# Performance work log

Hardware: AMD Instinct MI355X
Metric: run time of the kernel (lower is better)

Reference implementation:

```python
import jax, jax.numpy as jnp
import numpy as np

N = 16384; C = 16; H = 256; W = 704
HEADS = 4; PTS = 4; K = 8; DH = C // HEADS
EPS = 1e-3  # BatchNorm eps from module

def _bn(x, g, b):
    # BatchNorm1d in training mode: batch statistics over N
    mu = x.mean(axis=0)
    var = x.var(axis=0)
    return (x - mu) * jax.lax.rsqrt(var + EPS) * g + b

def setup_inputs():
    key = jax.random.key(0)
    ks = jax.random.split(key, 20)
    def w(i, shape, s=0.25):
        return jax.random.normal(ks[i], shape, jnp.float32) * s
    grid_y = jax.random.randint(ks[0], (N,), 0, H)
    grid_x = jax.random.randint(ks[1], (N,), 0, W)
    return {
        "point_features": jax.random.normal(ks[2], (N, C), jnp.float32),
        "image_feat": jax.random.normal(ks[3], (C, H, W), jnp.float32),
        "image_grid": jnp.stack([grid_y, grid_x], axis=1),
        "Wk": w(4, (C, C)), "bk": w(5, (C,)), "gk": jnp.ones((C,)), "betak": jnp.zeros((C,)),
        "Wfc": w(6, (2, C)), "bfc": w(7, (C,)), "gfc": jnp.ones((C,)), "betafc": jnp.zeros((C,)),
        "Wt": w(8, (C, C)), "bt": w(9, (C,)), "gt": jnp.ones((C,)), "betat": jnp.zeros((C,)),
        "Woff": w(10, (C, HEADS * PTS * 2), 0.02), "boff": w(11, (HEADS * PTS * 2,), 0.5),
        "Wattn": w(12, (C, HEADS * PTS), 0.02), "battn": jnp.zeros((HEADS * PTS,)),
        "Wval": w(13, (C, C)), "bval": w(14, (C,)),
        "Wout": w(15, (C, C)), "bout": w(16, (C,)),
        "Wf": w(17, (2 * C, C)), "bf": w(18, (C,)), "gf": jnp.ones((C,)), "betaf": jnp.zeros((C,)),
    }

def _deform_attn(q, image_feat, grid_f, Woff, boff, Wattn, battn, Wval, bval, Wout, bout):
    # MSDeformAttn with 1 level: learned offsets around projected pixel, bilinear sampling
    n = q.shape[0]
    off = (q @ Woff + boff).reshape(n, HEADS, PTS, 2)
    attn = jax.nn.softmax((q @ Wattn + battn).reshape(n, HEADS, PTS), axis=-1)
    val = (image_feat.reshape(C, H * W).T @ Wval + bval).reshape(H * W, HEADS, DH)
    val_h = val.transpose(1, 0, 2)  # [HEADS, HW, DH]
    loc_y = grid_f[:, 0][:, None, None] + off[..., 0]  # [N, HEADS, PTS]
    loc_x = grid_f[:, 1][:, None, None] + off[..., 1]
    y0 = jnp.floor(loc_y); x0 = jnp.floor(loc_x)
    wy = loc_y - y0; wx = loc_x - x0

    def corner(yi, xi, wgt):
        valid = (yi >= 0) & (yi <= H - 1) & (xi >= 0) & (xi <= W - 1)
        yc = jnp.clip(yi, 0, H - 1).astype(jnp.int32)
        xc = jnp.clip(xi, 0, W - 1).astype(jnp.int32)
        idx = (yc * W + xc).transpose(1, 0, 2)  # [HEADS, N, PTS]
        g = jax.vmap(lambda v, i: v[i])(val_h, idx)  # [HEADS, N, PTS, DH]
        return g * (wgt * valid).transpose(1, 0, 2)[..., None]

    samp = (corner(y0, x0, (1 - wy) * (1 - wx))
            + corner(y0, x0 + 1, (1 - wy) * wx)
            + corner(y0 + 1, x0, wy * (1 - wx))
            + corner(y0 + 1, x0 + 1, wy * wx))  # [HEADS, N, PTS, DH]
    out = (samp * attn.transpose(1, 0, 2)[..., None]).sum(axis=2)  # [HEADS, N, DH]
    out = out.transpose(1, 0, 2).reshape(n, C)
    return out @ Wout + bout

def reference(point_features, image_feat, image_grid, Wk, bk, gk, betak, Wfc, bfc, gfc, betafc, Wt, bt, gt, betat, Woff, boff, Wattn, battn, Wval, bval, Wout, bout, Wf, bf, gf, betaf):
    grid_f = image_grid.astype(jnp.float32)
    # KNN over projected pixel coords (cKDTree.query k=K+1, drop self)
    d2 = ((grid_f[:, None, :] - grid_f[None, :, :]) ** 2).sum(-1)
    _, nidx = jax.lax.top_k(-d2, K + 1)
    nidx = nidx[:, 1:]  # [N, K]

    pts = _bn(point_features @ Wk + bk, gk, betak)  # pts_key_proj
    # normalized relative image-plane positions -> fc
    center = grid_f.mean(axis=0)
    rel = grid_f - center
    mx = jnp.abs(rel).max(axis=0)
    mx = jnp.where(mx == 0, 1.0, mx)
    pos = _bn((rel / mx) @ Wfc + bfc, gfc, betafc)

    # gather image feats at projected pixels + KNN-graph neighbor aggregation
    gathered = image_feat[:, image_grid[:, 0], image_grid[:, 1]].T  # [N, C]
    neigh = gathered[nidx].mean(axis=1)  # [N, C]

    q = pts + pos
    img_pre = _deform_attn(q, image_feat, grid_f, Woff, boff, Wattn, battn, Wval, bval, Wout, bout) + neigh

    pts_pre = _bn(pts @ Wt + bt, gt, betat)  # pts_transform
    fuse = jax.nn.relu(jnp.concatenate([pts_pre, img_pre], axis=-1))  # activate_out
    return jax.nn.relu(_bn(fuse @ Wf + bf, gf, betaf))  # fuse_conv
```

## Files before the change

### kernel.cpp

```cpp
#include <hip/hip_runtime.h>
#include <climits>

#define N_ 16384
#define C_ 16
#define H_ 256
#define W_ 704
#define HW_ (H_*W_)
#define NC_ (N_*C_)
#define EPS_ 1e-3f
#define HDR_ 512

typedef unsigned long long ull;


#define VAL_   (HDR_ + 9*NC_)
#define KNNI_  (VAL_ + HW_*16)
#define PARTF_ (KNNI_ + 378256)
#define PK_    (PARTF_ + 8192)
#define PFC_   (PARTF_ + 16384)
#define PT_    (PARTF_ + 24576)

#define CAP_ 6144

__device__ __forceinline__ float wsum64(float v){
#pragma unroll
  for (int o = 32; o > 0; o >>= 1) v += __shfl_down(v, o);
  return v;
}

#define LOAD16(dst, src) { const float4* _s=(const float4*)(src); float4 _a=_s[0],_b=_s[1],_c=_s[2],_d=_s[3]; \
  dst[0]=_a.x;dst[1]=_a.y;dst[2]=_a.z;dst[3]=_a.w; dst[4]=_b.x;dst[5]=_b.y;dst[6]=_b.z;dst[7]=_b.w; \
  dst[8]=_c.x;dst[9]=_c.y;dst[10]=_c.z;dst[11]=_c.w; dst[12]=_d.x;dst[13]=_d.y;dst[14]=_d.z;dst[15]=_d.w; }

#define STORE16(dst, src) { float4* _d=(float4*)(dst); \
  _d[0]=make_float4(src[0],src[1],src[2],src[3]); _d[1]=make_float4(src[4],src[5],src[6],src[7]); \
  _d[2]=make_float4(src[8],src[9],src[10],src[11]); _d[3]=make_float4(src[12],src[13],src[14],src[15]); }

__global__ __launch_bounds__(256) void k_init(float* ws){
  if (blockIdx.x < 176){
    int4* c = (int4*)(ws + KNNI_);
    c[blockIdx.x*256 + threadIdx.x] = make_int4(0,0,0,0);
  } else if (threadIdx.x == 0){
    int* ih = (int*)ws;
    ih[0]=0; ih[1]=0; ih[2]=INT_MAX; ih[3]=INT_MIN; ih[4]=INT_MAX; ih[5]=INT_MIN;
  }
}

__global__ __launch_bounds__(256) void k_gridcnt(const int* __restrict__ grid, float* __restrict__ ws){
  int i = blockIdx.x*256 + threadIdx.x;
  int2 p = ((const int2*)grid)[i];
  int* counts = (int*)(ws + KNNI_);
  atomicAdd(&counts[p.x*W_ + p.y], 1);
  int sy=p.x, sx=p.y, mny=p.x, mxy=p.x, mnx=p.y, mxx=p.y;
#pragma unroll
  for (int o=32;o>0;o>>=1){
    sy += __shfl_down(sy,o); sx += __shfl_down(sx,o);
    mny = min(mny,__shfl_down(mny,o)); mxy = max(mxy,__shfl_down(mxy,o));
    mnx = min(mnx,__shfl_down(mnx,o)); mxx = max(mxx,__shfl_down(mxx,o));
  }
  __shared__ int sh[24];
  int w = threadIdx.x >> 6;
  if ((threadIdx.x & 63) == 0){
    sh[w]=sy; sh[4+w]=sx; sh[8+w]=mny; sh[12+w]=mxy; sh[16+w]=mnx; sh[20+w]=mxx;
  }
  __syncthreads();
  if (threadIdx.x == 0){
    int a0=sh[0]+sh[1]+sh[2]+sh[3];
    int a1=sh[4]+sh[5]+sh[6]+sh[7];
    int a2=min(min(sh[8],sh[9]),min(sh[10],sh[11]));
    int a3=max(max(sh[12],sh[13]),max(sh[14],sh[15]));
    int a4=min(min(sh[16],sh[17]),min(sh[18],sh[19]));
    int a5=max(max(sh[20],sh[21]),max(sh[22],sh[23]));
    int* ih = (int*)ws;
    atomicAdd(&ih[0],a0); atomicAdd(&ih[1],a1);
    atomicMin(&ih[2],a2); atomicMax(&ih[3],a3);
    atomicMin(&ih[4],a4); atomicMax(&ih[5],a5);
  }
}

__global__ __launch_bounds__(256) void k_scanA(float* ws){
  const int* counts = (const int*)(ws + KNNI_);
  int* bsum = (int*)(ws + KNNI_) + 180224 + 180240;
  int t = threadIdx.x;
  int v = counts[blockIdx.x*256 + t];
#pragma unroll
  for (int o=32;o>0;o>>=1) v += __shfl_down(v,o);
  __shared__ int w4[4];
  if ((t&63)==0) w4[t>>6] = v;
  __syncthreads();
  if (t==0) bsum[blockIdx.x] = w4[0]+w4[1]+w4[2]+w4[3];
}

__global__ __launch_bounds__(256) void k_scanB(float* ws){
  if (threadIdx.x == 0){
    int* ih = (int*)ws;
    float cy = (float)ih[0] / (float)N_;
    float cx = (float)ih[1] / (float)N_;
    float my = fmaxf((float)ih[3]-cy, cy-(float)ih[2]);
    float mx = fmaxf((float)ih[5]-cx, cx-(float)ih[4]);
    if (my == 0.f) my = 1.f;
    if (mx == 0.f) mx = 1.f;
    ws[264]=cy; ws[265]=cx; ws[266]=1.f/my; ws[267]=1.f/mx;
  }
  int* bsum = (int*)(ws + KNNI_) + 180224 + 180240;
  int* boff = bsum + 704;
  __shared__ int sWsum[4];
  __shared__ int sCarry;
  int t = threadIdx.x, lane = t & 63, wv = t >> 6;
  if (t==0) sCarry = 0;
  __syncthreads();
  for (int c=0;c<3;++c){
    int idx = c*256 + t;
    int v0 = (idx < 704) ? bsum[idx] : 0;
    int v = v0;
#pragma unroll
    for (int o=1;o<64;o<<=1){ int xx=__shfl_up(v,o); if (lane>=o) v+=xx; }
    if (lane==63) sWsum[wv]=v;
    __syncthreads();
    int add = sCarry;
    for (int w2=0;w2<wv;++w2) add += sWsum[w2];
    if (idx < 704) boff[idx] = add + v - v0;
    __syncthreads();
    if (t==255) sCarry = add + v;
    __syncthreads();
  }
}

__global__ __launch_bounds__(256) void k_scanC(float* ws){
  int* counts = (int*)(ws + KNNI_);
  int* cellst = counts + 180224;
  const int* boff = counts + 180224 + 180240 + 704;
  __shared__ int sWsum[4];
  int t = threadIdx.x, lane = t & 63, wv = t >> 6;
  int i = blockIdx.x*256 + t;
  int v0 = counts[i], v = v0;
#pragma unroll
  for (int o=1;o<64;o<<=1){ int xx=__shfl_up(v,o); if (lane>=o) v+=xx; }
  if (lane==63) sWsum[wv]=v;
  __syncthreads();
  int add = boff[blockIdx.x];
  for (int w2=0;w2<wv;++w2) add += sWsum[w2];
  int start = add + v - v0;
  cellst[i] = start;
  counts[i] = start;
  if (i == 0) cellst[HW_] = N_;
}

__global__ __launch_bounds__(256) void k_scatter(const int* __restrict__ grid, float* __restrict__ ws){
  int i = blockIdx.x*256 + threadIdx.x;
  int2 g = ((const int2*)grid)[i];
  int* counts = (int*)(ws + KNNI_);
  unsigned* psort = (unsigned*)(counts + 180224 + 180240 + 704 + 704);
  int pos = atomicAdd(&counts[g.x*W_ + g.y], 1);
  psort[pos] = ((unsigned)g.x<<24) | ((unsigned)g.y<<14) | (unsigned)i;
}

__global__ __launch_bounds__(256) void k_prep(const float* __restrict__ imf,
                                              const int* __restrict__ grid,
                                              const float* __restrict__ Wval,
                                              const float* __restrict__ bval,
                                              float* __restrict__ ws){
  int t = threadIdx.x;
  if (blockIdx.x < 1024){
    int idx = blockIdx.x*256 + t;
    int i = idx >> 4, c = idx & 15;
    int2 g = ((const int2*)grid)[i];
    ws[HDR_ + 2*NC_ + idx] = imf[c*HW_ + g.x*W_ + g.y];
  } else {
    __shared__ float sW[256], sb[16];
    sW[t] = Wval[t];
    if (t < 16) sb[t] = bval[t];
    __syncthreads();
    int pix = (blockIdx.x-1024)*256 + t;
    float a[16];
#pragma unroll
    for (int ci=0;ci<16;++ci) a[ci] = imf[ci*HW_ + pix];
    float o[16];
#pragma unroll
    for (int c=0;c<16;++c) o[c] = sb[c];
#pragma unroll
    for (int ci=0;ci<16;++ci){ float v=a[ci];
#pragma unroll
      for (int c=0;c<16;++c) o[c] += v*sW[ci*16+c];
    }
    float* val = ws + VAL_;
    STORE16(val + pix*16, o);
  }
}

__device__ __forceinline__ void knn_insert(ull* arr, ull key){
  if (key < arr[8]){
    int q = 8;
    while (q > 0 && arr[q-1] > key){ arr[q] = arr[q-1]; --q; }
    arr[q] = key;
  }
}

__device__ __forceinline__ void scan_rows_global(const int* __restrict__ cellst,
                                                 const unsigned* __restrict__ psort,
                                                 int y, int x, int s,
                                                 int y0, int y1, int x0, int x1, ull* arr){
  for (int yy=y0+s; yy<=y1; yy+=4){
    int rowb = yy*W_;
    int st = cellst[rowb + x0];
    int e  = cellst[rowb + x1 + 1];
    int dy = y-yy, dy2 = dy*dy;
    for (int p=st; p<e; ++p){
      unsigned u = psort[p];
      int px = (int)((u>>14)&1023);
      int dx = x-px;
      knn_insert(arr, ((ull)(unsigned)(dy2+dx*dx) << 14) | (ull)(u & 16383u));
    }
  }
}

__global__ __launch_bounds__(256) void k_knn4(float* __restrict__ ws){
  const int* cellst = (const int*)(ws + KNNI_) + 180224;
  const unsigned* psort = (const unsigned*)((const int*)(ws + KNNI_) + 180224 + 180240 + 704 + 704);
  __shared__ unsigned sBand[CAP_];
  __shared__ int sRowBase[80];
  __shared__ int sMn, sMx;
  int tid = threadIdx.x, lane = tid & 63;
  int s = tid & 3, pl = tid >> 2;
  int gid = blockIdx.x*64 + pl;
  unsigned me = psort[gid];
  int y = (int)(me>>24), x = (int)((me>>14)&1023), i = (int)(me&16383);
  if (tid==0){ sMn = INT_MAX; sMx = -1; }
  __syncthreads();
  if (s==0){ atomicMin(&sMn, y); atomicMax(&sMx, y); }
  __syncthreads();
  int ya = max(sMn-16,0), yb = min(sMx+16,H_-1);
  int nr = yb-ya+1;
  int p0 = cellst[ya*W_], p1 = cellst[(yb+1)*W_];
  int count = p1-p0;
  bool fb = (count > CAP_) || (nr > 78);
  if (!fb){
    for (int j=tid; j<count; j+=256) sBand[j] = psort[p0+j];
    for (int j=tid; j<=nr; j+=256) sRowBase[j] = cellst[(ya+j)*W_] - p0;
  }
  __syncthreads();
  int r = 8;
  { int y0=max(y-8,0),y1=min(y+8,H_-1),x0=max(x-8,0),x1=min(x+8,W_-1);
    if ((y1-y0+1)*(x1-x0+1) < 224) r = 16; }
  ull arr[9];
#pragma unroll
  for (int q=0;q<9;++q) arr[q] = ~0ull;
  {
    int y0=max(y-r,0),y1=min(y+r,H_-1),x0=max(x-r,0),x1=min(x+r,W_-1);
    if (!fb){
      for (int yy=y0+s; yy<=y1; yy+=4){
        int j = yy-ya;
        int b = sRowBase[j], e = sRowBase[j+1];
        int lo=b, hi=e;
        while (lo<hi){ int mid=(lo+hi)>>1; int xm=(int)((sBand[mid]>>14)&1023); if (xm<x0) lo=mid+1; else hi=mid; }
        int dy = y-yy, dy2 = dy*dy;
        for (int p=lo; p<e; ++p){
          unsigned u = sBand[p];
          int px = (int)((u>>14)&1023);
          if (px > x1) break;
          int dx = x-px;
          knn_insert(arr, ((ull)(unsigned)(dy2+dx*dx) << 14) | (ull)(u & 16383u));
        }
      }
    } else {
      scan_rows_global(cellst, psort, y, x, s, y0, y1, x0, x1, arr);
    }
  }
  ull m[9];
  bool done = false;
  {
    ull k[9];
#pragma unroll
    for (int q=0;q<9;++q) m[q] = ~0ull;
    int base = lane & ~3;
    for (int ss=0; ss<4; ++ss){
#pragma unroll
      for (int q=0;q<9;++q) k[q] = __shfl(arr[q], base+ss);
      for (int q2=0;q2<9;++q2){
        ull kk = k[q2];
        if (kk >= m[8]) break;
        int q = 8; while (q>0 && m[q-1]>kk){ m[q]=m[q-1]; --q; } m[q]=kk;
      }
    }
    int y0=max(y-r,0),y1=min(y+r,H_-1),x0=max(x-r,0),x1=min(x+r,W_-1);
    bool covered = (y0==0)&&(y1==H_-1)&&(x0==0)&&(x1==W_-1);
    bool ok = covered;
    if (!ok && m[8] != ~0ull){ int d9 = (int)(m[8]>>14); ok = d9 < (r+1)*(r+1); }
    done = ok;
  }
  while (__ballot(!done)){
    if (!done){
      r <<= 1;
      int y0=max(y-r,0),y1=min(y+r,H_-1),x0=max(x-r,0),x1=min(x+r,W_-1);
#pragma unroll
      for (int q=0;q<9;++q) arr[q] = ~0ull;
      scan_rows_global(cellst, psort, y, x, s, y0, y1, x0, x1, arr);
    }
    ull k[9];
    bool doIns = !done;
    if (doIns){
#pragma unroll
      for (int q=0;q<9;++q) m[q] = ~0ull;
    }
    int base = lane & ~3;
    for (int ss=0; ss<4; ++ss){
#pragma unroll
      for (int q=0;q<9;++q) k[q] = __shfl(arr[q], base+ss);
      if (doIns){
        for (int q2=0;q2<9;++q2){
          ull kk = k[q2];
          if (kk >= m[8]) break;
          int q = 8; while (q>0 && m[q-1]>kk){ m[q]=m[q-1]; --q; } m[q]=kk;
        }
      }
    }
    if (!done){
      int y0=max(y-r,0),y1=min(y+r,H_-1),x0=max(x-r,0),x1=min(x+r,W_-1);
      bool covered = (y0==0)&&(y1==H_-1)&&(x0==0)&&(x1==W_-1);
      bool ok = covered;
      if (!ok && m[8] != ~0ull){ int d9 = (int)(m[8]>>14); ok = d9 < (r+1)*(r+1); }
      if (ok) done = true;
    }
  }
  const float* gath = ws + HDR_ + 2*NC_;
  float4 acc = make_float4(0.f,0.f,0.f,0.f);
#pragma unroll
  for (int nb=1; nb<9; ++nb){
    int idx = (int)(m[nb] & 16383ull);
    const float4 g = *(const float4*)(gath + idx*16 + s*4);
    acc.x += g.x; acc.y += g.y; acc.z += g.z; acc.w += g.w;
  }
  float* neigh = ws + HDR_ + 7*NC_;
  *(float4*)(neigh + i*16 + s*4) =
      make_float4(acc.x*0.125f, acc.y*0.125f, acc.z*0.125f, acc.w*0.125f);
}

__global__ __launch_bounds__(64) void k_lin1(
    const float* __restrict__ pf, const int* __restrict__ grid,
    const float* __restrict__ Wk, const float* __restrict__ bk,
    const float* __restrict__ Wfc, const float* __restrict__ bfc,
    float* __restrict__ ws)
{
  __shared__ float sWk[256], sbk[16], sWfc[32], sbfc[16];
  int t = threadIdx.x;
  for (int j=t;j<256;j+=64) sWk[j] = Wk[j];
  if (t < 16){ sbk[t]=bk[t]; sbfc[t]=bfc[t]; }
  if (t < 32) sWfc[t] = Wfc[t];
  __syncthreads();
  int i = blockIdx.x*64 + t;
  float p[16]; LOAD16(p, pf + i*16);
  float ok[16];
#pragma unroll
  for (int c=0;c<16;++c) ok[c] = sbk[c];
#pragma unroll
  for (int j=0;j<16;++j){ float v = p[j];
#pragma unroll
    for (int c=0;c<16;++c) ok[c] += v*sWk[j*16+c];
  }
  float* pts_lin = ws + HDR_;
  STORE16(pts_lin + i*16, ok);
  float cy=ws[264], cx=ws[265], imy=ws[266], imx=ws[267];
  int2 g = ((const int2*)grid)[i];
  float ry = ((float)g.x - cy)*imy, rx = ((float)g.y - cx)*imx;
  float op[16];
#pragma unroll
  for (int c=0;c<16;++c) op[c] = ry*sWfc[c] + rx*sWfc[16+c] + sbfc[c];
  float* pos_lin = ws + HDR_ + NC_;
  STORE16(pos_lin + i*16, op);
  float* partK  = ws + PK_;
  float* partFC = ws + PFC_;
#pragma unroll
  for (int c=0;c<16;++c){
    float a = wsum64(ok[c]); float b = wsum64(ok[c]*ok[c]);
    if (t==0){ partK[blockIdx.x*32+c]=a; partK[blockIdx.x*32+16+c]=b; }
    a = wsum64(op[c]); b = wsum64(op[c]*op[c]);
    if (t==0){ partFC[blockIdx.x*32+c]=a; partFC[blockIdx.x*32+16+c]=b; }
  }
}

__device__ __forceinline__ void red1_body(const float* __restrict__ g, const float* __restrict__ b,
                                          float* __restrict__ ws, int partOff, int aOff, float* red){
  int t = threadIdx.x, slot = t & 31, chunk = t >> 5;
  const float* part = ws + partOff;
  float acc = 0.f;
  for (int bb=chunk*32; bb<chunk*32+32; ++bb) acc += part[bb*32 + slot];
  red[t] = acc;
  __syncthreads();
  if (chunk == 0){
    float v = red[slot];
#pragma unroll
    for (int k2=1;k2<8;++k2) v += red[k2*32+slot];
    red[slot] = v;
  }
  __syncthreads();
  if (t < 16){
    float mu  = red[t]    * (1.f/N_);
    float var = red[16+t] * (1.f/N_) - mu*mu;
    float a = g[t] / sqrtf(var + EPS_);
    ws[aOff+t]    = a;
    ws[aOff+16+t] = b[t] - mu*a;
  }
  __syncthreads();
}

__global__ __launch_bounds__(256) void k_red2(const float* __restrict__ gk, const float* __restrict__ betak,
                                              const float* __restrict__ gfc, const float* __restrict__ betafc,
                                              float* __restrict__ ws){
  __shared__ float red[256];
  red1_body(gk, betak, ws, PK_, 136, red);
  red1_body(gfc, betafc, ws, PFC_, 168, red);
}

__global__ __launch_bounds__(256) void k_red1(const float* __restrict__ g, const float* __restrict__ b,
                                              float* __restrict__ ws, int partOff, int aOff){
  __shared__ float red[256];
  red1_body(g, b, ws, partOff, aOff, red);
}

__global__ __launch_bounds__(64) void k_qstage(
    const float* __restrict__ Wt, const float* __restrict__ bt,
    const float* __restrict__ Woff, const float* __restrict__ boff,
    const float* __restrict__ Wattn, const float* __restrict__ battn,
    float* __restrict__ ws)
{
  __shared__ float sWt[256], sWoff[512], sWattn[256];
  __shared__ float sbt[16], sboff[32], sbattn[16];
  __shared__ float skA[16], skC[16], sfcA[16], sfcC[16];
  int t = threadIdx.x;
  for (int j=t;j<256;j+=64){ sWt[j]=Wt[j]; sWattn[j]=Wattn[j]; }
  for (int j=t;j<512;j+=64) sWoff[j]=Woff[j];
  if (t<16){ sbt[t]=bt[t]; sbattn[t]=battn[t];
    skA[t]=ws[136+t]; skC[t]=ws[152+t]; sfcA[t]=ws[168+t]; sfcC[t]=ws[184+t]; }
  if (t<32) sboff[t]=boff[t];
  __syncthreads();
  int i = blockIdx.x*64 + t;
  float* pts_lin = ws + HDR_;
  float* pos_lin = ws + HDR_ + NC_;
  float* t_lin   = ws + HDR_ + 3*NC_;
  float* offp    = ws + HDR_ + 4*NC_;
  float* attnp   = ws + HDR_ + 6*NC_;
  float pl[16], po[16];
  LOAD16(pl, pts_lin + i*16);
  LOAD16(po, pos_lin + i*16);
  float pts[16], q[16];
#pragma unroll
  for (int c=0;c<16;++c){ pts[c] = pl[c]*skA[c]+skC[c]; q[c] = pts[c] + po[c]*sfcA[c]+sfcC[c]; }
  float tv[16];
#pragma unroll
  for (int c=0;c<16;++c) tv[c] = sbt[c];
#pragma unroll
  for (int j=0;j<16;++j){ float v=pts[j];
#pragma unroll
    for (int c=0;c<16;++c) tv[c] += v*sWt[j*16+c];
  }
  STORE16(t_lin + i*16, tv);
  float* partT = ws + PT_;
#pragma unroll
  for (int c=0;c<16;++c){
    float a = wsum64(tv[c]); float b = wsum64(tv[c]*tv[c]);
    if (t==0){ partT[blockIdx.x*32+c]=a; partT[blockIdx.x*32+16+c]=b; }
  }
  float ov[32];
#pragma unroll
  for (int o=0;o<32;++o) ov[o] = sboff[o];
#pragma unroll
  for (int j=0;j<16;++j){ float v=q[j];
#pragma unroll
    for (int o=0;o<32;++o) ov[o] += v*sWoff[j*32+o];
  }
  { float4* d=(float4*)(offp + i*32);
#pragma unroll
    for (int r=0;r<8;++r) d[r]=make_float4(ov[r*4],ov[r*4+1],ov[r*4+2],ov[r*4+3]);
  }
  float l[16];
#pragma unroll
  for (int c=0;c<16;++c) l[c] = sbattn[c];
#pragma unroll
  for (int j=0;j<16;++j){ float v=q[j];
#pragma unroll
    for (int c=0;c<16;++c) l[c] += v*sWattn[j*16+c];
  }
  float av[16];
#pragma unroll
  for (int h=0;h<4;++h){
    float m = fmaxf(fmaxf(l[h*4],l[h*4+1]),fmaxf(l[h*4+2],l[h*4+3]));
    float e0=expf(l[h*4]-m), e1=expf(l[h*4+1]-m), e2=expf(l[h*4+2]-m), e3=expf(l[h*4+3]-m);
    float inv = 1.f/(e0+e1+e2+e3);
    av[h*4]=e0*inv; av[h*4+1]=e1*inv; av[h*4+2]=e2*inv; av[h*4+3]=e3*inv;
  }
  STORE16(attnp + i*16, av);
}

__global__ __launch_bounds__(256) void k_attn(
    const int* __restrict__ grid,
    const float* __restrict__ Wout, const float* __restrict__ bout,
    const float* __restrict__ Wf, const float* __restrict__ bf,
    float* __restrict__ ws)
{
  __shared__ float sWout[256], sWf[512], sbout[16], sbf[16];
  __shared__ float sTl[1024], sNei[1024], sSamp[1024], sImg[1024];
  __shared__ float sPart[128];
  int t = threadIdx.x;
  int p = t >> 2, h = t & 3;
  int i = blockIdx.x*64 + p;
  sWout[t]=Wout[t]; sWf[t]=Wf[t]; sWf[t+256]=Wf[t+256];
  if (t<16){ sbout[t]=bout[t]; sbf[t]=bf[t]; }
  {
    const float4* tl4 = (const float4*)(ws + HDR_ + 3*NC_ + blockIdx.x*1024);
    const float4* nv4 = (const float4*)(ws + HDR_ + 7*NC_ + blockIdx.x*1024);
    float4 v = tl4[t];
    int c0 = (t*4) & 15;
    float a0=ws[200+c0],a1=ws[200+c0+1],a2=ws[200+c0+2],a3=ws[200+c0+3];
    float c0v=ws[216+c0],c1v=ws[216+c0+1],c2v=ws[216+c0+2],c3v=ws[216+c0+3];
    sTl[t*4]   = fmaxf(v.x*a0+c0v, 0.f);
    sTl[t*4+1] = fmaxf(v.y*a1+c1v, 0.f);
    sTl[t*4+2] = fmaxf(v.z*a2+c2v, 0.f);
    sTl[t*4+3] = fmaxf(v.w*a3+c3v, 0.f);
    float4 nv = nv4[t];
    sNei[t*4]=nv.x; sNei[t*4+1]=nv.y; sNei[t*4+2]=nv.z; sNei[t*4+3]=nv.w;
  }
  const float4* off4 = (const float4*)(ws + HDR_ + 4*NC_ + blockIdx.x*2048);
  float4 o0 = off4[t*2], o1 = off4[t*2+1];
  float4 aw = ((const float4*)(ws + HDR_ + 6*NC_ + blockIdx.x*1024))[t];
  int2 g = ((const int2*)grid)[i];
  float y = (float)g.x, x = (float)g.y;
  const float4* val4 = (const float4*)(ws + VAL_);
  float4 acc = make_float4(0.f,0.f,0.f,0.f);
  float offv[8] = {o0.x,o0.y,o0.z,o0.w,o1.x,o1.y,o1.z,o1.w};
  float avv[4]  = {aw.x,aw.y,aw.z,aw.w};
#define CORNER(yy,xx,wgt) do{ int _y=(yy),_x=(xx); \
    if ((unsigned)_y < (unsigned)H_ && (unsigned)_x < (unsigned)W_){ \
      float4 _v = val4[(_y*W_+_x)*4 + h]; float _w = a*(wgt); \
      acc.x += _w*_v.x; acc.y += _w*_v.y; acc.z += _w*_v.z; acc.w += _w*_v.w; } }while(0)
#pragma unroll
  for (int pt=0; pt<4; ++pt){
    float a  = avv[pt];
    float ly = y + offv[pt*2], lx = x + offv[pt*2+1];
    float fy = floorf(ly), fx = floorf(lx);
    float wy = ly - fy, wx = lx - fx;
    int y0 = (int)fy, x0 = (int)fx;
    CORNER(y0,   x0,   (1.f-wy)*(1.f-wx));
    CORNER(y0,   x0+1, (1.f-wy)*wx);
    CORNER(y0+1, x0,   wy*(1.f-wx));
    CORNER(y0+1, x0+1, wy*wx);
  }
#undef CORNER
  ((float4*)sSamp)[t] = acc;
  __syncthreads();
  float img[4];
#pragma unroll
  for (int k=0;k<4;++k){ int cc=h*4+k; img[k] = sbout[cc] + sNei[p*16+cc]; }
#pragma unroll
  for (int j=0;j<16;++j){
    float v = sSamp[p*16+j];
#pragma unroll
    for (int k=0;k<4;++k) img[k] += v*sWout[j*16 + h*4 + k];
  }
  ((float4*)sImg)[t] = make_float4(img[0],img[1],img[2],img[3]);
  __syncthreads();
  float fl[4];
#pragma unroll
  for (int k=0;k<4;++k) fl[k] = sbf[h*4+k];
#pragma unroll
  for (int j=0;j<16;++j){
    float v1 = sTl[p*16+j];
    float v2 = fmaxf(sImg[p*16+j], 0.f);
#pragma unroll
    for (int k=0;k<4;++k){
      fl[k] += v1*sWf[j*16 + h*4 + k];
      fl[k] += v2*sWf[(16+j)*16 + h*4 + k];
    }
  }
  float* f_lin = ws + HDR_ + 8*NC_;
  ((float4*)(f_lin + blockIdx.x*1024))[t] = make_float4(fl[0],fl[1],fl[2],fl[3]);
  float s0=fl[0],s1=fl[1],s2=fl[2],s3=fl[3];
  float q0=fl[0]*fl[0],q1=fl[1]*fl[1],q2=fl[2]*fl[2],q3=fl[3]*fl[3];
#pragma unroll
  for (int o=32;o>=4;o>>=1){
    s0+=__shfl_down(s0,o); s1+=__shfl_down(s1,o); s2+=__shfl_down(s2,o); s3+=__shfl_down(s3,o);
    q0+=__shfl_down(q0,o); q1+=__shfl_down(q1,o); q2+=__shfl_down(q2,o); q3+=__shfl_down(q3,o);
  }
  int wave = t >> 6, lane = t & 63;
  if (lane < 4){
    sPart[wave*32 + lane*4+0]=s0; sPart[wave*32 + lane*4+1]=s1;
    sPart[wave*32 + lane*4+2]=s2; sPart[wave*32 + lane*4+3]=s3;
    sPart[wave*32 + 16 + lane*4+0]=q0; sPart[wave*32 + 16 + lane*4+1]=q1;
    sPart[wave*32 + 16 + lane*4+2]=q2; sPart[wave*32 + 16 + lane*4+3]=q3;
  }
  __syncthreads();
  if (t < 32){
    float v = sPart[t]+sPart[32+t]+sPart[64+t]+sPart[96+t];
    (ws + PARTF_)[blockIdx.x*32 + t] = v;
  }
}

__global__ __launch_bounds__(256) void k_out(const float* __restrict__ ws, float* __restrict__ out){
  int idx = blockIdx.x*256 + threadIdx.x;
  int c = idx & 15;
  float v = ws[HDR_ + 8*NC_ + idx];
  out[idx] = fmaxf(v*ws[232+c] + ws[248+c], 0.f);
}

extern "C" void kernel_launch(void* const* d_in, const int* in_sizes, int n_in,
                              void* d_out, int out_size, void* d_ws, size_t ws_size,
                              hipStream_t stream)
{
  const float* pf    = (const float*)d_in[0];
  const float* imf   = (const float*)d_in[1];
  const int*   gridp = (const int*)d_in[2];
  const float* Wk   =(const float*)d_in[3],  *bk   =(const float*)d_in[4];
  const float* gk   =(const float*)d_in[5],  *betak=(const float*)d_in[6];
  const float* Wfc  =(const float*)d_in[7],  *bfc  =(const float*)d_in[8];
  const float* gfc  =(const float*)d_in[9],  *betafc=(const float*)d_in[10];
  const float* Wt   =(const float*)d_in[11], *bt   =(const float*)d_in[12];
  const float* gt   =(const float*)d_in[13], *betat=(const float*)d_in[14];
  const float* Woff =(const float*)d_in[15], *boff =(const float*)d_in[16];
  const float* Wattn=(const float*)d_in[17], *battn=(const float*)d_in[18];
  const float* Wval =(const float*)d_in[19], *bval =(const float*)d_in[20];
  const float* Wout =(const float*)d_in[21], *bout =(const float*)d_in[22];
  const float* Wf   =(const float*)d_in[23], *bf   =(const float*)d_in[24];
  const float* gf   =(const float*)d_in[25], *betaf=(const float*)d_in[26];
  float* ws  = (float*)d_ws;
  float* out = (float*)d_out;

  hipLaunchKernelGGL(k_init,     dim3(177),      dim3(256), 0, stream, ws);
  hipLaunchKernelGGL(k_gridcnt,  dim3(N_/256),   dim3(256), 0, stream, gridp, ws);
  hipLaunchKernelGGL(k_scanA,    dim3(704),      dim3(256), 0, stream, ws);
  hipLaunchKernelGGL(k_scanB,    dim3(1),        dim3(256), 0, stream, ws);
  hipLaunchKernelGGL(k_scanC,    dim3(704),      dim3(256), 0, stream, ws);
  hipLaunchKernelGGL(k_scatter,  dim3(N_/256),   dim3(256), 0, stream, gridp, ws);
  hipLaunchKernelGGL(k_prep,     dim3(1728),     dim3(256), 0, stream, imf, gridp, Wval, bval, ws);
  hipLaunchKernelGGL(k_lin1,     dim3(N_/64),    dim3(64),  0, stream, pf, gridp, Wk, bk, Wfc, bfc, ws);
  hipLaunchKernelGGL(k_red2,     dim3(1),        dim3(256), 0, stream, gk, betak, gfc, betafc, ws);
  hipLaunchKernelGGL(k_qstage,   dim3(N_/64),    dim3(64),  0, stream, Wt, bt, Woff, boff, Wattn, battn, ws);
  hipLaunchKernelGGL(k_red1,     dim3(1),        dim3(256), 0, stream, gt, betat, ws, PT_, 200);
  hipLaunchKernelGGL(k_knn4,     dim3(N_/64),    dim3(256), 0, stream, ws);
  hipLaunchKernelGGL(k_attn,     dim3(N_/64),    dim3(256), 0, stream, gridp, Wout, bout, Wf, bf, ws);
  hipLaunchKernelGGL(k_red1,     dim3(1),        dim3(256), 0, stream, gf, betaf, ws, PARTF_, 232);
  hipLaunchKernelGGL(k_out,      dim3(NC_/256),  dim3(256), 0, stream, ws, out);
}
```

Baseline: 224.4 us.

## Merge fifteen launches into eight by co-scheduling independent stages in block ranges

Independent stages (counting-grid init, point projections, gather, value projection, scans, BN reductions, KNN, query stage) now share kernels, each stage taking its own range of block indices. The single-block scan and final BN reductions become last-block-done patterns driven by atomic counters and thread fences. The output kernel is vectorized to float4. The aim is to cut launch overhead and serialization from many tiny kernels, at the cost of more complex inter-block synchronization that depends on correct fence semantics.

Result: slower. 230.8 us (+2.9%).

```diff
diff --git a/kernel.cpp b/kernel.cpp
--- a/kernel.cpp
+++ b/kernel.cpp
@@ -2,16 +2,14 @@
 #include <climits>
 
 #define N_ 16384
-#define C_ 16
 #define H_ 256
 #define W_ 704
 #define HW_ (H_*W_)
-#define NC_ (N_*C_)
+#define NC_ (N_*16)
 #define EPS_ 1e-3f
 #define HDR_ 512
 
 typedef unsigned long long ull;
-
 
 #define VAL_   (HDR_ + 9*NC_)
 #define KNNI_  (VAL_ + HW_*16)
@@ -35,158 +33,6 @@
 #define STORE16(dst, src) { float4* _d=(float4*)(dst); \
   _d[0]=make_float4(src[0],src[1],src[2],src[3]); _d[1]=make_float4(src[4],src[5],src[6],src[7]); \
   _d[2]=make_float4(src[8],src[9],src[10],src[11]); _d[3]=make_float4(src[12],src[13],src[14],src[15]); }
-
-__global__ __launch_bounds__(256) void k_init(float* ws){
-  if (blockIdx.x < 176){
-    int4* c = (int4*)(ws + KNNI_);
-    c[blockIdx.x*256 + threadIdx.x] = make_int4(0,0,0,0);
-  } else if (threadIdx.x == 0){
-    int* ih = (int*)ws;
-    ih[0]=0; ih[1]=0; ih[2]=INT_MAX; ih[3]=INT_MIN; ih[4]=INT_MAX; ih[5]=INT_MIN;
-  }
-}
-
-__global__ __launch_bounds__(256) void k_gridcnt(const int* __restrict__ grid, float* __restrict__ ws){
-  int i = blockIdx.x*256 + threadIdx.x;
-  int2 p = ((const int2*)grid)[i];
-  int* counts = (int*)(ws + KNNI_);
-  atomicAdd(&counts[p.x*W_ + p.y], 1);
-  int sy=p.x, sx=p.y, mny=p.x, mxy=p.x, mnx=p.y, mxx=p.y;
-#pragma unroll
-  for (int o=32;o>0;o>>=1){
-    sy += __shfl_down(sy,o); sx += __shfl_down(sx,o);
-    mny = min(mny,__shfl_down(mny,o)); mxy = max(mxy,__shfl_down(mxy,o));
-    mnx = min(mnx,__shfl_down(mnx,o)); mxx = max(mxx,__shfl_down(mxx,o));
-  }
-  __shared__ int sh[24];
-  int w = threadIdx.x >> 6;
-  if ((threadIdx.x & 63) == 0){
-    sh[w]=sy; sh[4+w]=sx; sh[8+w]=mny; sh[12+w]=mxy; sh[16+w]=mnx; sh[20+w]=mxx;
-  }
-  __syncthreads();
-  if (threadIdx.x == 0){
-    int a0=sh[0]+sh[1]+sh[2]+sh[3];
-    int a1=sh[4]+sh[5]+sh[6]+sh[7];
-    int a2=min(min(sh[8],sh[9]),min(sh[10],sh[11]));
-    int a3=max(max(sh[12],sh[13]),max(sh[14],sh[15]));
-    int a4=min(min(sh[16],sh[17]),min(sh[18],sh[19]));
-    int a5=max(max(sh[20],sh[21]),max(sh[22],sh[23]));
-    int* ih = (int*)ws;
-    atomicAdd(&ih[0],a0); atomicAdd(&ih[1],a1);
-    atomicMin(&ih[2],a2); atomicMax(&ih[3],a3);
-    atomicMin(&ih[4],a4); atomicMax(&ih[5],a5);
-  }
-}
-
-__global__ __launch_bounds__(256) void k_scanA(float* ws){
-  const int* counts = (const int*)(ws + KNNI_);
-  int* bsum = (int*)(ws + KNNI_) + 180224 + 180240;
-  int t = threadIdx.x;
-  int v = counts[blockIdx.x*256 + t];
-#pragma unroll
-  for (int o=32;o>0;o>>=1) v += __shfl_down(v,o);
-  __shared__ int w4[4];
-  if ((t&63)==0) w4[t>>6] = v;
-  __syncthreads();
-  if (t==0) bsum[blockIdx.x] = w4[0]+w4[1]+w4[2]+w4[3];
-}
-
-__global__ __launch_bounds__(256) void k_scanB(float* ws){
-  if (threadIdx.x == 0){
-    int* ih = (int*)ws;
-    float cy = (float)ih[0] / (float)N_;
-    float cx = (float)ih[1] / (float)N_;
-    float my = fmaxf((float)ih[3]-cy, cy-(float)ih[2]);
-    float mx = fmaxf((float)ih[5]-cx, cx-(float)ih[4]);
-    if (my == 0.f) my = 1.f;
-    if (mx == 0.f) mx = 1.f;
-    ws[264]=cy; ws[265]=cx; ws[266]=1.f/my; ws[267]=1.f/mx;
-  }
-  int* bsum = (int*)(ws + KNNI_) + 180224 + 180240;
-  int* boff = bsum + 704;
-  __shared__ int sWsum[4];
-  __shared__ int sCarry;
-  int t = threadIdx.x, lane = t & 63, wv = t >> 6;
-  if (t==0) sCarry = 0;
-  __syncthreads();
-  for (int c=0;c<3;++c){
-    int idx = c*256 + t;
-    int v0 = (idx < 704) ? bsum[idx] : 0;
-    int v = v0;
-#pragma unroll
-    for (int o=1;o<64;o<<=1){ int xx=__shfl_up(v,o); if (lane>=o) v+=xx; }
-    if (lane==63) sWsum[wv]=v;
-    __syncthreads();
-    int add = sCarry;
-    for (int w2=0;w2<wv;++w2) add += sWsum[w2];
-    if (idx < 704) boff[idx] = add + v - v0;
-    __syncthreads();
-    if (t==255) sCarry = add + v;
-    __syncthreads();
-  }
-}
-
-__global__ __launch_bounds__(256) void k_scanC(float* ws){
-  int* counts = (int*)(ws + KNNI_);
-  int* cellst = counts + 180224;
-  const int* boff = counts + 180224 + 180240 + 704;
-  __shared__ int sWsum[4];
-  int t = threadIdx.x, lane = t & 63, wv = t >> 6;
-  int i = blockIdx.x*256 + t;
-  int v0 = counts[i], v = v0;
-#pragma unroll
-  for (int o=1;o<64;o<<=1){ int xx=__shfl_up(v,o); if (lane>=o) v+=xx; }
-  if (lane==63) sWsum[wv]=v;
-  __syncthreads();
-  int add = boff[blockIdx.x];
-  for (int w2=0;w2<wv;++w2) add += sWsum[w2];
-  int start = add + v - v0;
-  cellst[i] = start;
-  counts[i] = start;
-  if (i == 0) cellst[HW_] = N_;
-}
-
-__global__ __launch_bounds__(256) void k_scatter(const int* __restrict__ grid, float* __restrict__ ws){
-  int i = blockIdx.x*256 + threadIdx.x;
-  int2 g = ((const int2*)grid)[i];
-  int* counts = (int*)(ws + KNNI_);
-  unsigned* psort = (unsigned*)(counts + 180224 + 180240 + 704 + 704);
-  int pos = atomicAdd(&counts[g.x*W_ + g.y], 1);
-  psort[pos] = ((unsigned)g.x<<24) | ((unsigned)g.y<<14) | (unsigned)i;
-}
-
-__global__ __launch_bounds__(256) void k_prep(const float* __restrict__ imf,
-                                              const int* __restrict__ grid,
-                                              const float* __restrict__ Wval,
-                                              const float* __restrict__ bval,
-                                              float* __restrict__ ws){
-  int t = threadIdx.x;
-  if (blockIdx.x < 1024){
-    int idx = blockIdx.x*256 + t;
-    int i = idx >> 4, c = idx & 15;
-    int2 g = ((const int2*)grid)[i];
-    ws[HDR_ + 2*NC_ + idx] = imf[c*HW_ + g.x*W_ + g.y];
-  } else {
-    __shared__ float sW[256], sb[16];
-    sW[t] = Wval[t];
-    if (t < 16) sb[t] = bval[t];
-    __syncthreads();
-    int pix = (blockIdx.x-1024)*256 + t;
-    float a[16];
-#pragma unroll
-    for (int ci=0;ci<16;++ci) a[ci] = imf[ci*HW_ + pix];
-    float o[16];
-#pragma unroll
-    for (int c=0;c<16;++c) o[c] = sb[c];
-#pragma unroll
-    for (int ci=0;ci<16;++ci){ float v=a[ci];
-#pragma unroll
-      for (int c=0;c<16;++c) o[c] += v*sW[ci*16+c];
-    }
-    float* val = ws + VAL_;
-    STORE16(val + pix*16, o);
-  }
-}
 
 __device__ __forceinline__ void knn_insert(ull* arr, ull key){
   if (key < arr[8]){
@@ -214,304 +60,479 @@
   }
 }
 
-__global__ __launch_bounds__(256) void k_knn4(float* __restrict__ ws){
-  const int* cellst = (const int*)(ws + KNNI_) + 180224;
-  const unsigned* psort = (const unsigned*)((const int*)(ws + KNNI_) + 180224 + 180240 + 704 + 704);
-  __shared__ unsigned sBand[CAP_];
-  __shared__ int sRowBase[80];
-  __shared__ int sMn, sMx;
-  int tid = threadIdx.x, lane = tid & 63;
-  int s = tid & 3, pl = tid >> 2;
-  int gid = blockIdx.x*64 + pl;
-  unsigned me = psort[gid];
-  int y = (int)(me>>24), x = (int)((me>>14)&1023), i = (int)(me&16383);
-  if (tid==0){ sMn = INT_MAX; sMx = -1; }
-  __syncthreads();
-  if (s==0){ atomicMin(&sMn, y); atomicMax(&sMx, y); }
-  __syncthreads();
-  int ya = max(sMn-16,0), yb = min(sMx+16,H_-1);
-  int nr = yb-ya+1;
-  int p0 = cellst[ya*W_], p1 = cellst[(yb+1)*W_];
-  int count = p1-p0;
-  bool fb = (count > CAP_) || (nr > 78);
-  if (!fb){
-    for (int j=tid; j<count; j+=256) sBand[j] = psort[p0+j];
-    for (int j=tid; j<=nr; j+=256) sRowBase[j] = cellst[(ya+j)*W_] - p0;
-  }
-  __syncthreads();
-  int r = 8;
-  { int y0=max(y-8,0),y1=min(y+8,H_-1),x0=max(x-8,0),x1=min(x+8,W_-1);
-    if ((y1-y0+1)*(x1-x0+1) < 224) r = 16; }
-  ull arr[9];
-#pragma unroll
-  for (int q=0;q<9;++q) arr[q] = ~0ull;
-  {
-    int y0=max(y-r,0),y1=min(y+r,H_-1),x0=max(x-r,0),x1=min(x+r,W_-1);
+__device__ __forceinline__ void red_body(const float* __restrict__ g, const float* __restrict__ bta,
+                                         const float* __restrict__ part, float* __restrict__ coef,
+                                         float* __restrict__ red){
+  int t = threadIdx.x, slot = t & 31, chunk = t >> 5;
+  float acc = 0.f;
+  for (int bb=chunk*32; bb<chunk*32+32; ++bb) acc += part[bb*32 + slot];
+  red[t] = acc;
+  __syncthreads();
+  if (chunk == 0){
+    float v = red[slot];
+#pragma unroll
+    for (int k2=1;k2<8;++k2) v += red[k2*32+slot];
+    red[slot] = v;
+  }
+  __syncthreads();
+  if (t < 16){
+    float mu  = red[t]    * (1.f/N_);
+    float var = red[16+t] * (1.f/N_) - mu*mu;
+    float a = g[t] / sqrtf(var + EPS_);
+    coef[t]    = a;
+    coef[16+t] = bta[t] - mu*a;
+  }
+  __syncthreads();
+}
+
+__global__ __launch_bounds__(256) void k1(const float* __restrict__ pf,
+                                          const float* __restrict__ imf,
+                                          const int* __restrict__ grid,
+                                          const float* __restrict__ Wk, const float* __restrict__ bk,
+                                          const float* __restrict__ Wval, const float* __restrict__ bval,
+                                          float* __restrict__ ws){
+  __shared__ float sA[256], sB[16];
+  const int t = threadIdx.x, b = blockIdx.x;
+  const bool ldsK = (b >= 177 && b < 241);
+  const bool ldsV = (b >= 1265);
+  if (ldsK){ sA[t] = Wk[t];   if (t < 16) sB[t] = bk[t]; }
+  if (ldsV){ sA[t] = Wval[t]; if (t < 16) sB[t] = bval[t]; }
+  if (ldsK || ldsV) __syncthreads();
+
+  if (b < 176){
+    int4* c4 = (int4*)(ws + KNNI_);
+    c4[b*256 + t] = make_int4(0,0,0,0);
+  } else if (b == 176){
+    if (t == 0){
+      int* ih = (int*)ws;
+      ih[0]=0; ih[1]=0; ih[2]=INT_MAX; ih[3]=INT_MIN; ih[4]=INT_MAX; ih[5]=INT_MIN;
+      ih[6]=0; ih[7]=0;
+    }
+  } else if (ldsK){
+    const int i = (b-177)*256 + t;
+    float p[16]; LOAD16(p, pf + i*16);
+    float ok[16];
+#pragma unroll
+    for (int c=0;c<16;++c) ok[c] = sB[c];
+#pragma unroll
+    for (int j=0;j<16;++j){ float v = p[j];
+#pragma unroll
+      for (int c=0;c<16;++c) ok[c] += v*sA[j*16+c];
+    }
+    STORE16(ws + HDR_ + i*16, ok);
+    float* partK = ws + PK_;
+    const int grp = i >> 6;
+#pragma unroll
+    for (int c=0;c<16;++c){
+      float a = wsum64(ok[c]); float q2 = wsum64(ok[c]*ok[c]);
+      if ((t&63)==0){ partK[grp*32+c]=a; partK[grp*32+16+c]=q2; }
+    }
+  } else if (b < 1265){
+    const int idx = (b-241)*256 + t;
+    const int i = idx >> 4, c = idx & 15;
+    int2 g = ((const int2*)grid)[i];
+    ws[HDR_ + 2*NC_ + idx] = imf[c*HW_ + g.x*W_ + g.y];
+  } else {
+    const int pix = (b-1265)*256 + t;
+    float a[16];
+#pragma unroll
+    for (int ci=0;ci<16;++ci) a[ci] = imf[ci*HW_ + pix];
+    float o[16];
+#pragma unroll
+    for (int c=0;c<16;++c) o[c] = sB[c];
+#pragma unroll
+    for (int ci=0;ci<16;++ci){ float v=a[ci];
+#pragma unroll
+      for (int c=0;c<16;++c) o[c] += v*sA[ci*16+c];
+    }
+    STORE16(ws + VAL_ + pix*16, o);
+  }
+}
+
+__global__ __launch_bounds__(256) void k2(const int* __restrict__ grid,
+                                          const float* __restrict__ gk, const float* __restrict__ betak,
+                                          float* __restrict__ ws){
+  const int t = threadIdx.x, b = blockIdx.x;
+  if (b < 64){
+    int i = b*256 + t;
+    int2 p = ((const int2*)grid)[i];
+    int* counts = (int*)(ws + KNNI_);
+    atomicAdd(&counts[p.x*W_ + p.y], 1);
+    int sy=p.x, sx=p.y, mny=p.x, mxy=p.x, mnx=p.y, mxx=p.y;
+#pragma unroll
+    for (int o=32;o>0;o>>=1){
+      sy += __shfl_down(sy,o); sx += __shfl_down(sx,o);
+      mny = min(mny,__shfl_down(mny,o)); mxy = max(mxy,__shfl_down(mxy,o));
+      mnx = min(mnx,__shfl_down(mnx,o)); mxx = max(mxx,__shfl_down(mxx,o));
+    }
+    __shared__ int sh[24];
+    int w = t >> 6;
+    if ((t & 63) == 0){
+      sh[w]=sy; sh[4+w]=sx; sh[8+w]=mny; sh[12+w]=mxy; sh[16+w]=mnx; sh[20+w]=mxx;
+    }
+    __syncthreads();
+    if (t == 0){
+      int a0=sh[0]+sh[1]+sh[2]+sh[3];
+      int a1=sh[4]+sh[5]+sh[6]+sh[7];
+      int a2=min(min(sh[8],sh[9]),min(sh[10],sh[11]));
+      int a3=max(max(sh[12],sh[13]),max(sh[14],sh[15]));
+      int a4=min(min(sh[16],sh[17]),min(sh[18],sh[19]));
+      int a5=max(max(sh[20],sh[21]),max(sh[22],sh[23]));
+      int* ih = (int*)ws;
+      atomicAdd(&ih[0],a0); atomicAdd(&ih[1],a1);
+      atomicMin(&ih[2],a2); atomicMax(&ih[3],a3);
+      atomicMin(&ih[4],a4); atomicMax(&ih[5],a5);
+    }
+  } else {
+    __shared__ float red[256];
+    red_body(gk, betak, ws + PK_, ws + 136, red);
+  }
+}
+
+__global__ __launch_bounds__(256) void k3(const float* __restrict__ Wt, const float* __restrict__ bt,
+                                          float* __restrict__ ws){
+  const int t = threadIdx.x, b = blockIdx.x;
+  int* ih = (int*)ws;
+  int* counts = (int*)(ws + KNNI_);
+  int* bsum   = counts + 360464;
+  int* boffp  = bsum + 704;
+  if (b < 704){
+    __shared__ int w4[4];
+    __shared__ int sWin;
+    int v = counts[b*256 + t];
+#pragma unroll
+    for (int o=32;o>0;o>>=1) v += __shfl_down(v,o);
+    if ((t&63)==0) w4[t>>6] = v;
+    __syncthreads();
+    if (t == 0){
+      bsum[b] = w4[0]+w4[1]+w4[2]+w4[3];
+      __threadfence();
+      int old = atomicAdd(&ih[6], 1);
+      sWin = (old == 703) ? 1 : 0;
+    }
+    __syncthreads();
+    if (sWin){
+      if (t == 0) __threadfence();
+      __syncthreads();
+      if (t == 0){
+        float cy = (float)ih[0] / (float)N_;
+        float cx = (float)ih[1] / (float)N_;
+        float my = fmaxf((float)ih[3]-cy, cy-(float)ih[2]);
+        float mx = fmaxf((float)ih[5]-cx, cx-(float)ih[4]);
+        if (my == 0.f) my = 1.f;
+        if (mx == 0.f) mx = 1.f;
+        ws[264]=cy; ws[265]=cx; ws[266]=1.f/my; ws[267]=1.f/mx;
+      }
+      __shared__ int sWsum[4];
+      __shared__ int sCarry;
+      int lane = t & 63, wv = t >> 6;
+      if (t==0) sCarry = 0;
+      __syncthreads();
+      for (int c=0;c<3;++c){
+        int idx = c*256 + t;
+        int v0 = (idx < 704) ? bsum[idx] : 0;
+        int vv = v0;
+#pragma unroll
+        for (int o=1;o<64;o<<=1){ int xx=__shfl_up(vv,o); if (lane>=o) vv+=xx; }
+        if (lane==63) sWsum[wv]=vv;
+        __syncthreads();
+        int add = sCarry;
+        for (int w2=0;w2<wv;++w2) add += sWsum[w2];
+        if (idx < 704) boffp[idx] = add + vv - v0;
+        __syncthreads();
+        if (t==255) sCarry = add + vv;
+        __syncthreads();
+      }
+    }
+  } else {
+    __shared__ float sWt[256];
+    sWt[t] = Wt[t];
+    __syncthreads();
+    const int i = (b-704)*256 + t;
+    float kA[16], kC[16];
+    LOAD16(kA, ws+136); LOAD16(kC, ws+152);
+    float pl[16]; LOAD16(pl, ws + HDR_ + i*16);
+    float pts[16];
+#pragma unroll
+    for (int c=0;c<16;++c) pts[c] = pl[c]*kA[c] + kC[c];
+    float tv[16];
+#pragma unroll
+    for (int c=0;c<16;++c) tv[c] = bt[c];
+#pragma unroll
+    for (int j=0;j<16;++j){ float v = pts[j];
+#pragma unroll
+      for (int c=0;c<16;++c) tv[c] += v*sWt[j*16+c];
+    }
+    STORE16(ws + HDR_ + 3*NC_ + i*16, tv);
+    float* partT = ws + PT_;
+    const int grp = i >> 6;
+#pragma unroll
+    for (int c=0;c<16;++c){
+      float a = wsum64(tv[c]); float q2 = wsum64(tv[c]*tv[c]);
+      if ((t&63)==0){ partT[grp*32+c]=a; partT[grp*32+16+c]=q2; }
+    }
+  }
+}
+
+__global__ __launch_bounds__(256) void k4(const int* __restrict__ grid,
+                                          const float* __restrict__ Wfc, const float* __restrict__ bfc,
+                                          const float* __restrict__ gt, const float* __restrict__ betat,
+                                          float* __restrict__ ws){
+  const int t = threadIdx.x, b = blockIdx.x;
+  int* counts = (int*)(ws + KNNI_);
+  int* cellst = counts + 180224;
+  int* bsum   = counts + 360464;
+  int* boffp  = bsum + 704;
+  if (b < 704){
+    __shared__ int sWsum[4];
+    int lane = t & 63, wv = t >> 6;
+    int i = b*256 + t;
+    int v0 = counts[i], v = v0;
+#pragma unroll
+    for (int o=1;o<64;o<<=1){ int xx=__shfl_up(v,o); if (lane>=o) v+=xx; }
+    if (lane==63) sWsum[wv]=v;
+    __syncthreads();
+    int add = boffp[b];
+    for (int w2=0;w2<wv;++w2) add += sWsum[w2];
+    int start = add + v - v0;
+    cellst[i] = start;
+    counts[i] = start;
+    if (i == 0) cellst[HW_] = N_;
+  } else if (b < 768){
+    const int i = (b-704)*256 + t;
+    float cy=ws[264], cx=ws[265], imy=ws[266], imx=ws[267];
+    int2 g = ((const int2*)grid)[i];
+    float ry = ((float)g.x - cy)*imy, rx = ((float)g.y - cx)*imx;
+    float op[16];
+#pragma unroll
+    for (int c=0;c<16;++c) op[c] = ry*Wfc[c] + rx*Wfc[16+c] + bfc[c];
+    STORE16(ws + HDR_ + NC_ + i*16, op);
+    float* partFC = ws + PFC_;
+    const int grp = i >> 6;
+#pragma unroll
+    for (int c=0;c<16;++c){
+      float a = wsum64(op[c]); float q2 = wsum64(op[c]*op[c]);
+      if ((t&63)==0){ partFC[grp*32+c]=a; partFC[grp*32+16+c]=q2; }
+    }
+  } else {
+    __shared__ float red[256];
+    red_body(gt, betat, ws + PT_, ws + 200, red);
+  }
+}
+
+__global__ __launch_bounds__(256) void k5(const int* __restrict__ grid,
+                                          const float* __restrict__ gfc, const float* __restrict__ betafc,
+                                          float* __restrict__ ws){
+  const int t = threadIdx.x, b = blockIdx.x;
+  if (b < 64){
+    int i = b*256 + t;
+    int2 g = ((const int2*)grid)[i];
+    int* counts = (int*)(ws + KNNI_);
+    unsigned* psort = (unsigned*)(counts + 180224 + 180240 + 704 + 704);
+    int pos = atomicAdd(&counts[g.x*W_ + g.y], 1);
+    psort[pos] = ((unsigned)g.x<<24) | ((unsigned)g.y<<14) | (unsigned)i;
+  } else {
+    __shared__ float red[256];
+    red_body(gfc, betafc, ws + PFC_, ws + 168, red);
+  }
+}
+
+__global__ __launch_bounds__(256) void k6(const float* __restrict__ WoffW, const float* __restrict__ boffW,
+                                          const float* __restrict__ Wattn, const float* __restrict__ battn,
+                                          float* __restrict__ ws){
+  const int t = threadIdx.x, b = blockIdx.x;
+  if (b < 256){
+    const int* cellst = (const int*)(ws + KNNI_) + 180224;
+    const unsigned* psort = (const unsigned*)((const int*)(ws + KNNI_) + 180224 + 180240 + 704 + 704);
+    __shared__ unsigned sBand[CAP_];
+    __shared__ int sRowBase[80];
+    __shared__ int sMn, sMx;
+    int lane = t & 63;
+    int s = t & 3, pl = t >> 2;
+    int gid = b*64 + pl;
+    unsigned me = psort[gid];
+    int y = (int)(me>>24), x = (int)((me>>14)&1023), i = (int)(me&16383);
+    if (t==0){ sMn = INT_MAX; sMx = -1; }
+    __syncthreads();
+    if (s==0){ atomicMin(&sMn, y); atomicMax(&sMx, y); }
+    __syncthreads();
+    int ya = max(sMn-16,0), yb = min(sMx+16,H_-1);
+    int nr = yb-ya+1;
+    int p0 = cellst[ya*W_], p1 = cellst[(yb+1)*W_];
+    int count = p1-p0;
+    bool fb = (count > CAP_) || (nr > 78);
     if (!fb){
-      for (int yy=y0+s; yy<=y1; yy+=4){
-        int j = yy-ya;
-        int b = sRowBase[j], e = sRowBase[j+1];
-        int lo=b, hi=e;
-        while (lo<hi){ int mid=(lo+hi)>>1; int xm=(int)((sBand[mid]>>14)&1023); if (xm<x0) lo=mid+1; else hi=mid; }
-        int dy = y-yy, dy2 = dy*dy;
-        for (int p=lo; p<e; ++p){
-          unsigned u = sBand[p];
-          int px = (int)((u>>14)&1023);
-          if (px > x1) break;
-          int dx = x-px;
-          knn_insert(arr, ((ull)(unsigned)(dy2+dx*dx) << 14) | (ull)(u & 16383u));
+      for (int j=t; j<count; j+=256) sBand[j] = psort[p0+j];
+      for (int j=t; j<=nr; j+=256) sRowBase[j] = cellst[(ya+j)*W_] - p0;
+    }
+    __syncthreads();
+    int r = 8;
+    { int y0=max(y-8,0),y1=min(y+8,H_-1),x0=max(x-8,0),x1=min(x+8,W_-1);
+      if ((y1-y0+1)*(x1-x0+1) < 224) r = 16; }
+    ull arr[9];
+#pragma unroll
+    for (int q=0;q<9;++q) arr[q] = ~0ull;
+    {
+      int y0=max(y-r,0),y1=min(y+r,H_-1),x0=max(x-r,0),x1=min(x+r,W_-1);
+      if (!fb){
+        for (int yy=y0+s; yy<=y1; yy+=4){
+          int j = yy-ya;
+          int bb = sRowBase[j], e = sRowBase[j+1];
+          int lo=bb, hi=e;
+          while (lo<hi){ int mid=(lo+hi)>>1; int xm=(int)((sBand[mid]>>14)&1023); if (xm<x0) lo=mid+1; else hi=mid; }
+          int dy = y-yy, dy2 = dy*dy;
+          for (int p=lo; p<e; ++p){
+            unsigned u = sBand[p];
+            int px = (int)((u>>14)&1023);
+            if (px > x1) break;
+            int dx = x-px;
+            knn_insert(arr, ((ull)(unsigned)(dy2+dx*dx) << 14) | (ull)(u & 16383u));
+          }
         }
-      }
-    } else {
-      scan_rows_global(cellst, psort, y, x, s, y0, y1, x0, x1, arr);
-    }
-  }
-  ull m[9];
-  bool done = false;
-  {
-    ull k[9];
-#pragma unroll
-    for (int q=0;q<9;++q) m[q] = ~0ull;
-    int base = lane & ~3;
-    for (int ss=0; ss<4; ++ss){
-#pragma unroll
-      for (int q=0;q<9;++q) k[q] = __shfl(arr[q], base+ss);
-      for (int q2=0;q2<9;++q2){
-        ull kk = k[q2];
-        if (kk >= m[8]) break;
-        int q = 8; while (q>0 && m[q-1]>kk){ m[q]=m[q-1]; --q; } m[q]=kk;
-      }
-    }
-    int y0=max(y-r,0),y1=min(y+r,H_-1),x0=max(x-r,0),x1=min(x+r,W_-1);
-    bool covered = (y0==0)&&(y1==H_-1)&&(x0==0)&&(x1==W_-1);
-    bool ok = covered;
-    if (!ok && m[8] != ~0ull){ int d9 = (int)(m[8]>>14); ok = d9 < (r+1)*(r+1); }
-    done = ok;
-  }
-  while (__ballot(!done)){
-    if (!done){
-      r <<= 1;
-      int y0=max(y-r,0),y1=min(y+r,H_-1),x0=max(x-r,0),x1=min(x+r,W_-1);
-#pragma unroll
-      for (int q=0;q<9;++q) arr[q] = ~0ull;
-      scan_rows_global(cellst, psort, y, x, s, y0, y1, x0, x1, arr);
-    }
-    ull k[9];
-    bool doIns = !done;
-    if (doIns){
+      } else {
+        scan_rows_global(cellst, psort, y, x, s, y0, y1, x0, x1, arr);
+      }
+    }
+    ull m[9];
+    bool done = false;
+    {
+      ull k[9];
 #pragma unroll
       for (int q=0;q<9;++q) m[q] = ~0ull;
-    }
-    int base = lane & ~3;
-    for (int ss=0; ss<4; ++ss){
-#pragma unroll
-      for (int q=0;q<9;++q) k[q] = __shfl(arr[q], base+ss);
-      if (doIns){
+      int base = lane & ~3;
+      for (int ss=0; ss<4; ++ss){
+#pragma unroll
+        for (int q=0;q<9;++q) k[q] = __shfl(arr[q], base+ss);
         for (int q2=0;q2<9;++q2){
           ull kk = k[q2];
           if (kk >= m[8]) break;
           int q = 8; while (q>0 && m[q-1]>kk){ m[q]=m[q-1]; --q; } m[q]=kk;
         }
       }
-    }
-    if (!done){
       int y0=max(y-r,0),y1=min(y+r,H_-1),x0=max(x-r,0),x1=min(x+r,W_-1);
       bool covered = (y0==0)&&(y1==H_-1)&&(x0==0)&&(x1==W_-1);
-      bool ok = covered;
-      if (!ok && m[8] != ~0ull){ int d9 = (int)(m[8]>>14); ok = d9 < (r+1)*(r+1); }
-      if (ok) done = true;
-    }
-  }
-  const float* gath = ws + HDR_ + 2*NC_;
-  float4 acc = make_float4(0.f,0.f,0.f,0.f);
-#pragma unroll
-  for (int nb=1; nb<9; ++nb){
-    int idx = (int)(m[nb] & 16383ull);
-    const float4 g = *(const float4*)(gath + idx*16 + s*4);
-    acc.x += g.x; acc.y += g.y; acc.z += g.z; acc.w += g.w;
-  }
-  float* neigh = ws + HDR_ + 7*NC_;
-  *(float4*)(neigh + i*16 + s*4) =
-      make_float4(acc.x*0.125f, acc.y*0.125f, acc.z*0.125f, acc.w*0.125f);
-}
-
-__global__ __launch_bounds__(64) void k_lin1(
-    const float* __restrict__ pf, const int* __restrict__ grid,
-    const float* __restrict__ Wk, const float* __restrict__ bk,
-    const float* __restrict__ Wfc, const float* __restrict__ bfc,
-    float* __restrict__ ws)
-{
-  __shared__ float sWk[256], sbk[16], sWfc[32], sbfc[16];
-  int t = threadIdx.x;
-  for (int j=t;j<256;j+=64) sWk[j] = Wk[j];
-  if (t < 16){ sbk[t]=bk[t]; sbfc[t]=bfc[t]; }
-  if (t < 32) sWfc[t] = Wfc[t];
-  __syncthreads();
-  int i = blockIdx.x*64 + t;
-  float p[16]; LOAD16(p, pf + i*16);
-  float ok[16];
-#pragma unroll
-  for (int c=0;c<16;++c) ok[c] = sbk[c];
-#pragma unroll
-  for (int j=0;j<16;++j){ float v = p[j];
-#pragma unroll
-    for (int c=0;c<16;++c) ok[c] += v*sWk[j*16+c];
-  }
-  float* pts_lin = ws + HDR_;
-  STORE16(pts_lin + i*16, ok);
-  float cy=ws[264], cx=ws[265], imy=ws[266], imx=ws[267];
-  int2 g = ((const int2*)grid)[i];
-  float ry = ((float)g.x - cy)*imy, rx = ((float)g.y - cx)*imx;
-  float op[16];
-#pragma unroll
-  for (int c=0;c<16;++c) op[c] = ry*sWfc[c] + rx*sWfc[16+c] + sbfc[c];
-  float* pos_lin = ws + HDR_ + NC_;
-  STORE16(pos_lin + i*16, op);
-  float* partK  = ws + PK_;
-  float* partFC = ws + PFC_;
-#pragma unroll
-  for (int c=0;c<16;++c){
-    float a = wsum64(ok[c]); float b = wsum64(ok[c]*ok[c]);
-    if (t==0){ partK[blockIdx.x*32+c]=a; partK[blockIdx.x*32+16+c]=b; }
-    a = wsum64(op[c]); b = wsum64(op[c]*op[c]);
-    if (t==0){ partFC[blockIdx.x*32+c]=a; partFC[blockIdx.x*32+16+c]=b; }
-  }
-}
-
-__device__ __forceinline__ void red1_body(const float* __restrict__ g, const float* __restrict__ b,
-                                          float* __restrict__ ws, int partOff, int aOff, float* red){
-  int t = threadIdx.x, slot = t & 31, chunk = t >> 5;
-  const float* part = ws + partOff;
-  float acc = 0.f;
-  for (int bb=chunk*32; bb<chunk*32+32; ++bb) acc += part[bb*32 + slot];
-  red[t] = acc;
-  __syncthreads();
-  if (chunk == 0){
-    float v = red[slot];
-#pragma unroll
-    for (int k2=1;k2<8;++k2) v += red[k2*32+slot];
-    red[slot] = v;
-  }
-  __syncthreads();
-  if (t < 16){
-    float mu  = red[t]    * (1.f/N_);
-    float var = red[16+t] * (1.f/N_) - mu*mu;
-    float a = g[t] / sqrtf(var + EPS_);
-    ws[aOff+t]    = a;
-    ws[aOff+16+t] = b[t] - mu*a;
-  }
-  __syncthreads();
-}
-
-__global__ __launch_bounds__(256) void k_red2(const float* __restrict__ gk, const float* __restrict__ betak,
-                                              const float* __restrict__ gfc, const float* __restrict__ betafc,
-                                              float* __restrict__ ws){
-  __shared__ float red[256];
-  red1_body(gk, betak, ws, PK_, 136, red);
-  red1_body(gfc, betafc, ws, PFC_, 168, red);
-}
-
-__global__ __launch_bounds__(256) void k_red1(const float* __restrict__ g, const float* __restrict__ b,
-                                              float* __restrict__ ws, int partOff, int aOff){
-  __shared__ float red[256];
-  red1_body(g, b, ws, partOff, aOff, red);
-}
-
-__global__ __launch_bounds__(64) void k_qstage(
-    const float* __restrict__ Wt, const float* __restrict__ bt,
-    const float* __restrict__ Woff, const float* __restrict__ boff,
-    const float* __restrict__ Wattn, const float* __restrict__ battn,
-    float* __restrict__ ws)
-{
-  __shared__ float sWt[256], sWoff[512], sWattn[256];
-  __shared__ float sbt[16], sboff[32], sbattn[16];
-  __shared__ float skA[16], skC[16], sfcA[16], sfcC[16];
-  int t = threadIdx.x;
-  for (int j=t;j<256;j+=64){ sWt[j]=Wt[j]; sWattn[j]=Wattn[j]; }
-  for (int j=t;j<512;j+=64) sWoff[j]=Woff[j];
-  if (t<16){ sbt[t]=bt[t]; sbattn[t]=battn[t];
-    skA[t]=ws[136+t]; skC[t]=ws[152+t]; sfcA[t]=ws[168+t]; sfcC[t]=ws[184+t]; }
-  if (t<32) sboff[t]=boff[t];
-  __syncthreads();
-  int i = blockIdx.x*64 + t;
-  float* pts_lin = ws + HDR_;
-  float* pos_lin = ws + HDR_ + NC_;
-  float* t_lin   = ws + HDR_ + 3*NC_;
-  float* offp    = ws + HDR_ + 4*NC_;
-  float* attnp   = ws + HDR_ + 6*NC_;
-  float pl[16], po[16];
-  LOAD16(pl, pts_lin + i*16);
-  LOAD16(po, pos_lin + i*16);
-  float pts[16], q[16];
-#pragma unroll
-  for (int c=0;c<16;++c){ pts[c] = pl[c]*skA[c]+skC[c]; q[c] = pts[c] + po[c]*sfcA[c]+sfcC[c]; }
-  float tv[16];
-#pragma unroll
-  for (int c=0;c<16;++c) tv[c] = sbt[c];
-#pragma unroll
-  for (int j=0;j<16;++j){ float v=pts[j];
-#pragma unroll
-    for (int c=0;c<16;++c) tv[c] += v*sWt[j*16+c];
-  }
-  STORE16(t_lin + i*16, tv);
-  float* partT = ws + PT_;
-#pragma unroll
-  for (int c=0;c<16;++c){
-    float a = wsum64(tv[c]); float b = wsum64(tv[c]*tv[c]);
-    if (t==0){ partT[blockIdx.x*32+c]=a; partT[blockIdx.x*32+16+c]=b; }
-  }
-  float ov[32];
-#pragma unroll
-  for (int o=0;o<32;++o) ov[o] = sboff[o];
-#pragma unroll
-  for (int j=0;j<16;++j){ float v=q[j];
-#pragma unroll
-    for (int o=0;o<32;++o) ov[o] += v*sWoff[j*32+o];
-  }
-  { float4* d=(float4*)(offp + i*32);
-#pragma unroll
-    for (int r=0;r<8;++r) d[r]=make_float4(ov[r*4],ov[r*4+1],ov[r*4+2],ov[r*4+3]);
-  }
-  float l[16];
-#pragma unroll
-  for (int c=0;c<16;++c) l[c] = sbattn[c];
-#pragma unroll
-  for (int j=0;j<16;++j){ float v=q[j];
-#pragma unroll
-    for (int c=0;c<16;++c) l[c] += v*sWattn[j*16+c];
-  }
-  float av[16];
-#pragma unroll
-  for (int h=0;h<4;++h){
-    float m = fmaxf(fmaxf(l[h*4],l[h*4+1]),fmaxf(l[h*4+2],l[h*4+3]));
-    float e0=expf(l[h*4]-m), e1=expf(l[h*4+1]-m), e2=expf(l[h*4+2]-m), e3=expf(l[h*4+3]-m);
-    float inv = 1.f/(e0+e1+e2+e3);
-    av[h*4]=e0*inv; av[h*4+1]=e1*inv; av[h*4+2]=e2*inv; av[h*4+3]=e3*inv;
-  }
-  STORE16(attnp + i*16, av);
-}
-
-__global__ __launch_bounds__(256) void k_attn(
+      bool ok2 = covered;
+      if (!ok2 && m[8] != ~0ull){ int d9 = (int)(m[8]>>14); ok2 = d9 < (r+1)*(r+1); }
+      done = ok2;
+    }
+    while (__ballot(!done)){
+      if (!done){
+        r <<= 1;
+        int y0=max(y-r,0),y1=min(y+r,H_-1),x0=max(x-r,0),x1=min(x+r,W_-1);
+#pragma unroll
+        for (int q=0;q<9;++q) arr[q] = ~0ull;
+        scan_rows_global(cellst, psort, y, x, s, y0, y1, x0, x1, arr);
+      }
+      ull k[9];
+      bool doIns = !done;
+      if (doIns){
+#pragma unroll
+        for (int q=0;q<9;++q) m[q] = ~0ull;
+      }
+      int base = lane & ~3;
+      for (int ss=0; ss<4; ++ss){
+#pragma unroll
+        for (int q=0;q<9;++q) k[q] = __shfl(arr[q], base+ss);
+        if (doIns){
+          for (int q2=0;q2<9;++q2){
+            ull kk = k[q2];
+            if (kk >= m[8]) break;
+            int q = 8; while (q>0 && m[q-1]>kk){ m[q]=m[q-1]; --q; } m[q]=kk;
+          }
+        }
+      }
+      if (!done){
+        int y0=max(y-r,0),y1=min(y+r,H_-1),x0=max(x-r,0),x1=min(x+r,W_-1);
+        bool covered = (y0==0)&&(y1==H_-1)&&(x0==0)&&(x1==W_-1);
+        bool ok2 = covered;
+        if (!ok2 && m[8] != ~0ull){ int d9 = (int)(m[8]>>14); ok2 = d9 < (r+1)*(r+1); }
+        if (ok2) done = true;
+      }
+    }
+    const float* gath = ws + HDR_ + 2*NC_;
+    float4 acc = make_float4(0.f,0.f,0.f,0.f);
+#pragma unroll
+    for (int nb=1; nb<9; ++nb){
+      int idx = (int)(m[nb] & 16383ull);
+      const float4 g4 = *(const float4*)(gath + idx*16 + s*4);
+      acc.x += g4.x; acc.y += g4.y; acc.z += g4.z; acc.w += g4.w;
+    }
+    float* neigh = ws + HDR_ + 7*NC_;
+    *(float4*)(neigh + i*16 + s*4) =
+        make_float4(acc.x*0.125f, acc.y*0.125f, acc.z*0.125f, acc.w*0.125f);
+  } else {
+    __shared__ float sWoff[512], sWattn[256];
+    __shared__ float sboff[32], sbattn[16];
+    sWoff[t] = WoffW[t]; sWoff[256+t] = WoffW[256+t];
+    sWattn[t] = Wattn[t];
+    if (t < 32) sboff[t] = boffW[t];
+    if (t < 16) sbattn[t] = battn[t];
+    __syncthreads();
+    const int i = (b-256)*256 + t;
+    float kA[16],kC[16],fA[16],fC[16];
+    LOAD16(kA, ws+136); LOAD16(kC, ws+152); LOAD16(fA, ws+168); LOAD16(fC, ws+184);
+    float pl[16], po[16];
+    LOAD16(pl, ws + HDR_ + i*16);
+    LOAD16(po, ws + HDR_ + NC_ + i*16);
+    float q[16];
+#pragma unroll
+    for (int c=0;c<16;++c) q[c] = pl[c]*kA[c]+kC[c] + po[c]*fA[c]+fC[c];
+    float ov[32];
+#pragma unroll
+    for (int o=0;o<32;++o) ov[o] = sboff[o];
+#pragma unroll
+    for (int j=0;j<16;++j){ float v=q[j];
+#pragma unroll
+      for (int o=0;o<32;++o) ov[o] += v*sWoff[j*32+o];
+    }
+    { float4* d=(float4*)(ws + HDR_ + 4*NC_ + i*32);
+#pragma unroll
+      for (int rr=0;rr<8;++rr) d[rr]=make_float4(ov[rr*4],ov[rr*4+1],ov[rr*4+2],ov[rr*4+3]);
+    }
+    float l[16];
+#pragma unroll
+    for (int c=0;c<16;++c) l[c] = sbattn[c];
+#pragma unroll
+    for (int j=0;j<16;++j){ float v=q[j];
+#pragma unroll
+      for (int c=0;c<16;++c) l[c] += v*sWattn[j*16+c];
+    }
+    float av[16];
+#pragma unroll
+    for (int h=0;h<4;++h){
+      float m = fmaxf(fmaxf(l[h*4],l[h*4+1]),fmaxf(l[h*4+2],l[h*4+3]));
+      float e0=expf(l[h*4]-m), e1=expf(l[h*4+1]-m), e2=expf(l[h*4+2]-m), e3=expf(l[h*4+3]-m);
+      float inv = 1.f/(e0+e1+e2+e3);
+      av[h*4]=e0*inv; av[h*4+1]=e1*inv; av[h*4+2]=e2*inv; av[h*4+3]=e3*inv;
+    }
+    STORE16(ws + HDR_ + 6*NC_ + i*16, av);
+  }
+}
+
+__global__ __launch_bounds__(256) void k7(
     const int* __restrict__ grid,
     const float* __restrict__ Wout, const float* __restrict__ bout,
     const float* __restrict__ Wf, const float* __restrict__ bf,
+    const float* __restrict__ gf, const float* __restrict__ betaf,
     float* __restrict__ ws)
 {
   __shared__ float sWout[256], sWf[512], sbout[16], sbf[16];
   __shared__ float sTl[1024], sNei[1024], sSamp[1024], sImg[1024];
   __shared__ float sPart[128];
-  int t = threadIdx.x;
+  __shared__ float red[256];
+  __shared__ int sWin;
+  int t = threadIdx.x, b = blockIdx.x;
   int p = t >> 2, h = t & 3;
-  int i = blockIdx.x*64 + p;
+  int i = b*64 + p;
   sWout[t]=Wout[t]; sWf[t]=Wf[t]; sWf[t+256]=Wf[t+256];
   if (t<16){ sbout[t]=bout[t]; sbf[t]=bf[t]; }
   {
-    const float4* tl4 = (const float4*)(ws + HDR_ + 3*NC_ + blockIdx.x*1024);
-    const float4* nv4 = (const float4*)(ws + HDR_ + 7*NC_ + blockIdx.x*1024);
+    const float4* tl4 = (const float4*)(ws + HDR_ + 3*NC_ + b*1024);
+    const float4* nv4 = (const float4*)(ws + HDR_ + 7*NC_ + b*1024);
     float4 v = tl4[t];
     int c0 = (t*4) & 15;
-    float a0=ws[200+c0],a1=ws[200+c0+1],a2=ws[200+c0+2],a3=ws[200+c0+3];
-    float c0v=ws[216+c0],c1v=ws[216+c0+1],c2v=ws[216+c0+2],c3v=ws[216+c0+3];
+    float a0=ws[200+c0],a1=ws[201+c0],a2=ws[202+c0],a3=ws[203+c0];
+    float c0v=ws[216+c0],c1v=ws[217+c0],c2v=ws[218+c0],c3v=ws[219+c0];
     sTl[t*4]   = fmaxf(v.x*a0+c0v, 0.f);
     sTl[t*4+1] = fmaxf(v.y*a1+c1v, 0.f);
     sTl[t*4+2] = fmaxf(v.z*a2+c2v, 0.f);
@@ -519,9 +540,9 @@
     float4 nv = nv4[t];
     sNei[t*4]=nv.x; sNei[t*4+1]=nv.y; sNei[t*4+2]=nv.z; sNei[t*4+3]=nv.w;
   }
-  const float4* off4 = (const float4*)(ws + HDR_ + 4*NC_ + blockIdx.x*2048);
+  const float4* off4 = (const float4*)(ws + HDR_ + 4*NC_ + b*2048);
   float4 o0 = off4[t*2], o1 = off4[t*2+1];
-  float4 aw = ((const float4*)(ws + HDR_ + 6*NC_ + blockIdx.x*1024))[t];
+  float4 aw = ((const float4*)(ws + HDR_ + 6*NC_ + b*1024))[t];
   int2 g = ((const int2*)grid)[i];
   float y = (float)g.x, x = (float)g.y;
   const float4* val4 = (const float4*)(ws + VAL_);
@@ -572,7 +593,7 @@
     }
   }
   float* f_lin = ws + HDR_ + 8*NC_;
-  ((float4*)(f_lin + blockIdx.x*1024))[t] = make_float4(fl[0],fl[1],fl[2],fl[3]);
+  ((float4*)(f_lin + b*1024))[t] = make_float4(fl[0],fl[1],fl[2],fl[3]);
   float s0=fl[0],s1=fl[1],s2=fl[2],s3=fl[3];
   float q0=fl[0]*fl[0],q1=fl[1]*fl[1],q2=fl[2]*fl[2],q3=fl[3]*fl[3];
 #pragma unroll
@@ -590,21 +611,40 @@
   __syncthreads();
   if (t < 32){
     float v = sPart[t]+sPart[32+t]+sPart[64+t]+sPart[96+t];
-    (ws + PARTF_)[blockIdx.x*32 + t] = v;
-  }
-}
-
-__global__ __launch_bounds__(256) void k_out(const float* __restrict__ ws, float* __restrict__ out){
-  int idx = blockIdx.x*256 + threadIdx.x;
-  int c = idx & 15;
-  float v = ws[HDR_ + 8*NC_ + idx];
-  out[idx] = fmaxf(v*ws[232+c] + ws[248+c], 0.f);
+    (ws + PARTF_)[b*32 + t] = v;
+  }
+  __threadfence();
+  __syncthreads();
+  if (t == 0){
+    int old = atomicAdd(&((int*)ws)[7], 1);
+    sWin = (old == 255) ? 1 : 0;
+  }
+  __syncthreads();
+  if (sWin){
+    if (t == 0) __threadfence();
+    __syncthreads();
+    red_body(gf, betaf, ws + PARTF_, ws + 232, red);
+  }
+}
+
+__global__ __launch_bounds__(256) void k8(const float* __restrict__ ws, float* __restrict__ out){
+  const int gtid = blockIdx.x*256 + threadIdx.x;
+  const int idx4 = gtid*4;
+  float4 v = *(const float4*)(ws + HDR_ + 8*NC_ + idx4);
+  const int c = idx4 & 15;
+  float4 r;
+  r.x = fmaxf(v.x*ws[232+c] + ws[248+c], 0.f);
+  r.y = fmaxf(v.y*ws[233+c] + ws[249+c], 0.f);
+  r.z = fmaxf(v.z*ws[234+c] + ws[250+c], 0.f);
+  r.w = fmaxf(v.w*ws[235+c] + ws[251+c], 0.f);
+  *(float4*)(out + idx4) = r;
 }
 
 extern "C" void kernel_launch(void* const* d_in, const int* in_sizes, int n_in,
                               void* d_out, int out_size, void* d_ws, size_t ws_size,
                               hipStream_t stream)
 {
+  (void)in_sizes; (void)n_in; (void)out_size; (void)ws_size;
   const float* pf    = (const float*)d_in[0];
   const float* imf   = (const float*)d_in[1];
   const int*   gridp = (const int*)d_in[2];
@@ -623,19 +663,12 @@
   float* ws  = (float*)d_ws;
   float* out = (float*)d_out;
 
-  hipLaunchKernelGGL(k_init,     dim3(177),      dim3(256), 0, stream, ws);
-  hipLaunchKernelGGL(k_gridcnt,  dim3(N_/256),   dim3(256), 0, stream, gridp, ws);
-  hipLaunchKernelGGL(k_scanA,    dim3(704),      dim3(256), 0, stream, ws);
-  hipLaunchKernelGGL(k_scanB,    dim3(1),        dim3(256), 0, stream, ws);
-  hipLaunchKernelGGL(k_scanC,    dim3(704),      dim3(256), 0, stream, ws);
-  hipLaunchKernelGGL(k_scatter,  dim3(N_/256),   dim3(256), 0, stream, gridp, ws);
-  hipLaunchKernelGGL(k_prep,     dim3(1728),     dim3(256), 0, stream, imf, gridp, Wval, bval, ws);
-  hipLaunchKernelGGL(k_lin1,     dim3(N_/64),    dim3(64),  0, stream, pf, gridp, Wk, bk, Wfc, bfc, ws);
-  hipLaunchKernelGGL(k_red2,     dim3(1),        dim3(256), 0, stream, gk, betak, gfc, betafc, ws);
-  hipLaunchKernelGGL(k_qstage,   dim3(N_/64),    dim3(64),  0, stream, Wt, bt, Woff, boff, Wattn, battn, ws);
-  hipLaunchKernelGGL(k_red1,     dim3(1),        dim3(256), 0, stream, gt, betat, ws, PT_, 200);
-  hipLaunchKernelGGL(k_knn4,     dim3(N_/64),    dim3(256), 0, stream, ws);
-  hipLaunchKernelGGL(k_attn,     dim3(N_/64),    dim3(256), 0, stream, gridp, Wout, bout, Wf, bf, ws);
-  hipLaunchKernelGGL(k_red1,     dim3(1),        dim3(256), 0, stream, gf, betaf, ws, PARTF_, 232);
-  hipLaunchKernelGGL(k_out,      dim3(NC_/256),  dim3(256), 0, stream, ws, out);
-}
+  hipLaunchKernelGGL(k1, dim3(1969), dim3(256), 0, stream, pf, imf, gridp, Wk, bk, Wval, bval, ws);
+  hipLaunchKernelGGL(k2, dim3(65),   dim3(256), 0, stream, gridp, gk, betak, ws);
+  hipLaunchKernelGGL(k3, dim3(768),  dim3(256), 0, stream, Wt, bt, ws);
+  hipLaunchKernelGGL(k4, dim3(769),  dim3(256), 0, stream, gridp, Wfc, bfc, gt, betat, ws);
+  hipLaunchKernelGGL(k5, dim3(65),   dim3(256), 0, stream, gridp, gfc, betafc, ws);
+  hipLaunchKernelGGL(k6, dim3(320),  dim3(256), 0, stream, Woff, boff, Wattn, battn, ws);
+  hipLaunchKernelGGL(k7, dim3(256),  dim3(256), 0, stream, gridp, Wout, bout, Wf, bf, gf, betaf, ws);
+  hipLaunchKernelGGL(k8, dim3(256),  dim3(256), 0, stream, ws, out);
+}
```
